# Optimization experiments

Measured on AMD Instinct MI355X. Metric: run time of the kernel, lower is better.

## Reference

```python
import jax, jax.numpy as jnp
import numpy as np

B, S, D = 2, 2048, 1024
H, DH = 16, 64
N_CTX = 2048
IGNORE = -100000.0


def setup_inputs() -> dict:
    key = jax.random.key(0)
    ks = jax.random.split(key, 6)
    scale = 0.02
    return {
        "x": jax.random.normal(ks[0], (B, S, D), dtype=jnp.float32),
        "W_Q": jax.random.normal(ks[1], (H, DH, D), dtype=jnp.float32) * scale,
        "W_K": jax.random.normal(ks[2], (H, DH, D), dtype=jnp.float32) * scale,
        "W_V": jax.random.normal(ks[3], (H, DH, D), dtype=jnp.float32) * scale,
        "W_O": jax.random.normal(ks[4], (H, D, DH), dtype=jnp.float32) * scale,
        "b_Q": jnp.zeros((H, DH), dtype=jnp.float32),
        "b_K": jnp.zeros((H, DH), dtype=jnp.float32),
        "b_V": jnp.zeros((H, DH), dtype=jnp.float32),
        "b_O": jnp.zeros((D,), dtype=jnp.float32),
    }


def reference(x, W_Q, W_K, W_V, W_O, b_Q, b_K, b_V, b_O):
    attn_scale = jnp.sqrt(jnp.asarray(DH, dtype=x.dtype))
    # q,k,v: [batch, pos, head, d_head]
    q = jnp.einsum('ihm,bpm->bpih', W_Q, x) + b_Q
    k = jnp.einsum('ihm,bpm->bpih', W_K, x) + b_K
    v = jnp.einsum('ihm,bpm->bpih', W_V, x) + b_V
    # scores: [batch, head, q_pos, k_pos]
    attn_scores = jnp.einsum('bpih,bqih->bipq', q, k) / attn_scale
    # causal mask (pos_start=0, no kv cache)
    qs, ks_ = attn_scores.shape[-2], attn_scores.shape[-1]
    mask = jnp.tril(jnp.ones((qs, ks_), dtype=bool))
    attn_scores = jnp.where(mask, attn_scores, jnp.asarray(IGNORE, dtype=attn_scores.dtype))
    attn_matrix = jax.nn.softmax(attn_scores, axis=-1)
    # z: [batch, q_pos, head, d_head]
    z = jnp.einsum('bpih,biqp->bqih', v, attn_matrix)
    out = jnp.einsum('idh,bqih->bqd', W_O, z) + b_O
    return out
```

## Files before the change

kernel.cpp:

```cpp
#include <hip/hip_runtime.h>

typedef __bf16 bf16;
typedef __bf16 bf16x4 __attribute__((ext_vector_type(4)));
typedef __bf16 bf16x8 __attribute__((ext_vector_type(8)));
typedef float f32x4 __attribute__((ext_vector_type(4)));
typedef unsigned u32x4 __attribute__((ext_vector_type(4)));

#define AS1C(p) ((const __attribute__((address_space(1))) void*)(p))
#define AS3(p)  ((__attribute__((address_space(3))) void*)(p))

__device__ __forceinline__ void gld16(const bf16* gsrc, bf16* ldst) {
  __builtin_amdgcn_global_load_lds(AS1C(gsrc), AS3(ldst), 16, 0, 0);
}


__global__ void castx_kernel(const float* __restrict__ x, bf16* __restrict__ xb) {
  const int n4 = (4096 * 1024) / 4;
  for (int i = blockIdx.x * blockDim.x + threadIdx.x; i < n4; i += gridDim.x * blockDim.x) {
    float4 v = ((const float4*)x)[i];
    bf16x4 o;
    o[0] = (bf16)v.x; o[1] = (bf16)v.y; o[2] = (bf16)v.z; o[3] = (bf16)v.w;
    ((bf16x4*)xb)[i] = o;
  }
}

__global__ void prep_kernel(const float* __restrict__ WQ, const float* __restrict__ WK,
                            const float* __restrict__ WV, const float* __restrict__ WO,
                            const float* __restrict__ bQ, const float* __restrict__ bK,
                            const float* __restrict__ bV,
                            bf16* __restrict__ Wqkv, bf16* __restrict__ Wo2,
                            float* __restrict__ biasq) {
  const int WN = 1024 * 1024;
  const int total = 4 * WN + 3072;
  for (int i = blockIdx.x * blockDim.x + threadIdx.x; i < total; i += gridDim.x * blockDim.x) {
    if (i < WN) {
      Wqkv[i] = (bf16)(WQ[i] * 0.125f);
    } else if (i < 2 * WN) {
      Wqkv[i] = (bf16)WK[i - WN];
    } else if (i < 3 * WN) {
      Wqkv[i] = (bf16)WV[i - 2 * WN];
    } else if (i < 4 * WN) {
      int j = i - 3 * WN;
      int hh = j >> 16, r = j & 65535, d = r >> 6, dh = r & 63;
      Wo2[d * 1024 + hh * 64 + dh] = (bf16)WO[j];
    } else {
      int n = i - 4 * WN;
      biasq[n] = (n < 1024) ? bQ[n] * 0.125f : (n < 2048) ? bK[n - 1024] : bV[n - 2048];
    }
  }
}

template <int MODE>
__global__ __launch_bounds__(256)
void gemm_bt(const bf16* __restrict__ A, const bf16* __restrict__ Bw,
             const float* __restrict__ bias,
             bf16* __restrict__ Qo, bf16* __restrict__ Ko, bf16* __restrict__ Vt,
             float* __restrict__ Co, int M, int N, int K) {
  __shared__ bf16 As[128 * 64];
  __shared__ bf16 Bs[128 * 64];
  const int tid = threadIdx.x;
  const int lane = tid & 63, w = tid >> 6;
  const int wr = w >> 1, wc = w & 1;
  const int g = lane >> 4, lr = lane & 15;
  const int brow = blockIdx.x * 128, bcol = blockIdx.y * 128;

  f32x4 acc[4][4] = {};

  for (int k0 = 0; k0 < K; k0 += 64) {
#pragma unroll
    for (int it = 0; it < 4; ++it) {
      const int chunk = it * 4 + w;
      const int e = chunk * 64 + lane;
      const int row = e >> 3;
      const int c8 = (e & 7) << 3;
      gld16(A + (size_t)(brow + row) * K + k0 + c8, As + chunk * 512);
      gld16(Bw + (size_t)(bcol + row) * K + k0 + c8, Bs + chunk * 512);
    }
    __syncthreads();
#pragma unroll
    for (int kk = 0; kk < 2; ++kk) {
      bf16x8 af[4], bfm[4];
#pragma unroll
      for (int m = 0; m < 4; ++m)
        af[m] = *(const bf16x8*)(As + (wr * 64 + m * 16 + lr) * 64 + kk * 32 + g * 8);
#pragma unroll
      for (int n = 0; n < 4; ++n)
        bfm[n] = *(const bf16x8*)(Bs + (wc * 64 + n * 16 + lr) * 64 + kk * 32 + g * 8);
#pragma unroll
      for (int m = 0; m < 4; ++m)
#pragma unroll
        for (int n = 0; n < 4; ++n)
          acc[m][n] = __builtin_amdgcn_mfma_f32_16x16x32_bf16(af[m], bfm[n], acc[m][n], 0, 0, 0);
    }
    __syncthreads();
  }

  const int row0 = brow + wr * 64;
  const int col0 = bcol + wc * 64;
#pragma unroll
  for (int m = 0; m < 4; ++m) {
#pragma unroll
    for (int n = 0; n < 4; ++n) {
      const int nidx = col0 + n * 16 + lr;
      f32x4 v = acc[m][n];
      const float bs = bias[nidx];
      if (MODE == 0) {
        const int stream = nidx >> 10;
        const int j = nidx & 1023;
        const int hh = j >> 6, dh = j & 63;
        const int r0 = row0 + m * 16 + g * 4;
        const int b = r0 >> 11;
        const int p0 = r0 & 2047;
        if (stream == 2) {
          bf16x4 vv;
#pragma unroll
          for (int i = 0; i < 4; ++i) vv[i] = (bf16)(v[i] + bs);
          *(bf16x4*)(Vt + ((size_t)(b * 16 + hh) * 64 + dh) * 2048 + p0) = vv;
        } else {
          bf16* dst = (stream == 0) ? Qo : Ko;
#pragma unroll
          for (int i = 0; i < 4; ++i)
            dst[((size_t)(b * 16 + hh) * 2048 + (p0 + i)) * 64 + dh] = (bf16)(v[i] + bs);
        }
      } else {
#pragma unroll
        for (int i = 0; i < 4; ++i) {
          const int r = row0 + m * 16 + g * 4 + i;
          Co[(size_t)r * 1024 + nidx] = v[i] + bs;
        }
      }
    }
  }
}

__global__ __launch_bounds__(256, 4)
void attn_kernel(const bf16* __restrict__ Qm, const bf16* __restrict__ Km,
                 const bf16* __restrict__ Vm, bf16* __restrict__ Z) {
  const int nblk = blockIdx.x;
  const int xcd = nblk & 7, slot = nblk >> 3;
  const int G = ((slot >> 5) << 3) + xcd;
  const int qt = slot & 31;
  const int hh = G & 15, b = G >> 4;
  const int bh = b * 16 + hh;
  const int lane = threadIdx.x & 63, w = threadIdx.x >> 6;
  const int g = lane >> 4, lr = lane & 15;
  const bool g0 = g & 1, g1 = (g >> 1) & 1;

  __shared__ bf16 Ks[2][4096];
  __shared__ bf16 Vs[2][4096];

  const bf16* Qb = Qm + (size_t)bh * 2048 * 64;
  const bf16* Kb = Km + (size_t)bh * 2048 * 64;
  const bf16* Vb = Vm + (size_t)bh * 64 * 2048;

  auto stage = [&](int kv0, int bufi) {
#pragma unroll
    for (int it = 0; it < 2; ++it) {
      const int cb = w * 128 + it * 64;
      const int u = cb + lane;
      const int lc = u ^ ((u >> 3) & 7);
      const int row = lc >> 3, c8 = (lc & 7) * 8;
      gld16(Kb + (size_t)(kv0 + row) * 64 + c8, &Ks[bufi][cb * 8]);
      gld16(Vb + (size_t)row * 2048 + kv0 + c8, &Vs[bufi][cb * 8]);
    }
  };

  const int q0w = qt * 64 + w * 16;
  const int qg = q0w + lr;

  bf16x8 aq[2];
#pragma unroll
  for (int kk = 0; kk < 2; ++kk)
    aq[kk] = *(const bf16x8*)(Qb + (size_t)qg * 64 + kk * 32 + g * 8);

  float m_i = -1e30f, l_i = 0.f;
  f32x4 oacc[4] = {};

  stage(0, 0);
  __syncthreads();
  int buf = 0;

  for (int t = 0; t <= qt; ++t) {
    if (t < qt) stage((t + 1) * 64, buf ^ 1);
    const int kv0 = t * 64;

    f32x4 s[4] = {};
#pragma unroll
    for (int kk = 0; kk < 2; ++kk) {
#pragma unroll
      for (int n = 0; n < 4; ++n) {
        const int r = n * 16 + lr;
        const int sl = (r * 8 + kk * 4 + g) ^ (r & 7);
        bf16x8 bk = *(const bf16x8*)(&Ks[buf][sl * 8]);
        s[n] = __builtin_amdgcn_mfma_f32_16x16x32_bf16(bk, aq[kk], s[n], 0, 0, 0);
      }
    }
    if (t == qt) {
#pragma unroll
      for (int n = 0; n < 4; ++n)
#pragma unroll
        for (int i = 0; i < 4; ++i)
          if (kv0 + n * 16 + g * 4 + i > qg) s[n][i] = -1e9f;
    }

    float tm = fmaxf(fmaxf(fmaxf(s[0][0], s[0][1]), fmaxf(s[0][2], s[0][3])),
                     fmaxf(fmaxf(s[1][0], s[1][1]), fmaxf(s[1][2], s[1][3])));
    tm = fmaxf(tm, fmaxf(fmaxf(fmaxf(s[2][0], s[2][1]), fmaxf(s[2][2], s[2][3])),
                         fmaxf(fmaxf(s[3][0], s[3][1]), fmaxf(s[3][2], s[3][3]))));
    tm = fmaxf(tm, __shfl_xor(tm, 16));
    tm = fmaxf(tm, __shfl_xor(tm, 32));
    const float mn = fmaxf(m_i, tm);
    const float al = __expf(m_i - mn);
    m_i = mn;
#pragma unroll
    for (int n = 0; n < 4; ++n)
#pragma unroll
      for (int i = 0; i < 4; ++i) s[n][i] = __expf(s[n][i] - mn);
    float ts = ((s[0][0] + s[0][1]) + (s[0][2] + s[0][3])) +
               ((s[1][0] + s[1][1]) + (s[1][2] + s[1][3])) +
               ((s[2][0] + s[2][1]) + (s[2][2] + s[2][3])) +
               ((s[3][0] + s[3][1]) + (s[3][2] + s[3][3]));
    ts += __shfl_xor(ts, 16);
    ts += __shfl_xor(ts, 32);
    l_i = l_i * al + ts;
#pragma unroll
    for (int n = 0; n < 4; ++n)
#pragma unroll
      for (int i = 0; i < 4; ++i) oacc[n][i] *= al;

    unsigned U[8];
#pragma unroll
    for (int n = 0; n < 4; ++n)
#pragma unroll
      for (int h = 0; h < 2; ++h) {
        unsigned lo = (unsigned)__builtin_bit_cast(unsigned short, (bf16)s[n][2 * h]);
        unsigned hi = (unsigned)__builtin_bit_cast(unsigned short, (bf16)s[n][2 * h + 1]);
        U[n * 2 + h] = lo | (hi << 16);
      }
    unsigned rA0 = (unsigned)__shfl_xor((int)(g1 ? U[0] : U[2]), 32);
    unsigned rA1 = (unsigned)__shfl_xor((int)(g1 ? U[1] : U[3]), 32);
    unsigned rA2 = (unsigned)__shfl_xor((int)(g1 ? U[4] : U[6]), 32);
    unsigned rA3 = (unsigned)__shfl_xor((int)(g1 ? U[5] : U[7]), 32);
    unsigned v2_000 = g1 ? rA0 : U[0];
    unsigned v2_001 = g1 ? rA1 : U[1];
    unsigned v2_010 = g1 ? U[2] : rA0;
    unsigned v2_011 = g1 ? U[3] : rA1;
    unsigned v2_100 = g1 ? rA2 : U[4];
    unsigned v2_101 = g1 ? rA3 : U[5];
    unsigned v2_110 = g1 ? U[6] : rA2;
    unsigned v2_111 = g1 ? U[7] : rA3;
    unsigned rB0 = (unsigned)__shfl_xor((int)(g0 ? v2_000 : v2_010), 16);
    unsigned rB1 = (unsigned)__shfl_xor((int)(g0 ? v2_001 : v2_011), 16);
    unsigned rB2 = (unsigned)__shfl_xor((int)(g0 ? v2_100 : v2_110), 16);
    unsigned rB3 = (unsigned)__shfl_xor((int)(g0 ? v2_101 : v2_111), 16);
    u32x4 t0, t1;
    t0[0] = g0 ? rB0 : v2_000;
    t0[1] = g0 ? rB1 : v2_001;
    t0[2] = g0 ? v2_010 : rB0;
    t0[3] = g0 ? v2_011 : rB1;
    t1[0] = g0 ? rB2 : v2_100;
    t1[1] = g0 ? rB3 : v2_101;
    t1[2] = g0 ? v2_110 : rB2;
    t1[3] = g0 ? v2_111 : rB3;
    bf16x8 pb0 = __builtin_bit_cast(bf16x8, t0);
    bf16x8 pb1 = __builtin_bit_cast(bf16x8, t1);

#pragma unroll
    for (int kk = 0; kk < 2; ++kk) {
      const bf16x8 pb = kk ? pb1 : pb0;
#pragma unroll
      for (int n = 0; n < 4; ++n) {
        const int r = n * 16 + lr;
        const int sl = (r * 8 + kk * 4 + g) ^ (r & 7);
        bf16x8 av = *(const bf16x8*)(&Vs[buf][sl * 8]);
        oacc[n] = __builtin_amdgcn_mfma_f32_16x16x32_bf16(av, pb, oacc[n], 0, 0, 0);
      }
    }
    __syncthreads();
    buf ^= 1;
  }

  const float li = 1.f / l_i;
  bf16* zrow = Z + ((size_t)(b * 2048 + qg) * 16 + hh) * 64;
#pragma unroll
  for (int n = 0; n < 4; ++n) {
    bf16x4 o4;
#pragma unroll
    for (int i = 0; i < 4; ++i) o4[i] = (bf16)(oacc[n][i] * li);
    *(bf16x4*)(zrow + n * 16 + g * 4) = o4;
  }
}

extern "C" void kernel_launch(void* const* d_in, const int* in_sizes, int n_in,
                              void* d_out, int out_size, void* d_ws, size_t ws_size,
                              hipStream_t stream) {
  const float* x  = (const float*)d_in[0];
  const float* WQ = (const float*)d_in[1];
  const float* WK = (const float*)d_in[2];
  const float* WV = (const float*)d_in[3];
  const float* WO = (const float*)d_in[4];
  const float* bQ = (const float*)d_in[5];
  const float* bK = (const float*)d_in[6];
  const float* bV = (const float*)d_in[7];
  const float* bO = (const float*)d_in[8];
  float* out = (float*)d_out;

  char* ws = (char*)d_ws;
  bf16* xb    = (bf16*)(ws);
  bf16* Wqkv  = (bf16*)(ws + (8u << 20));
  bf16* Wo2   = (bf16*)(ws + (14u << 20));
  bf16* Qb    = (bf16*)(ws + (16u << 20));
  bf16* Kb    = (bf16*)(ws + (24u << 20));
  bf16* Vtb   = (bf16*)(ws + (32u << 20));
  bf16* Zb    = (bf16*)(ws + (40u << 20));
  float* biasq = (float*)(ws + (48u << 20));

  castx_kernel<<<2048, 256, 0, stream>>>(x, xb);
  prep_kernel<<<2048, 256, 0, stream>>>(WQ, WK, WV, WO, bQ, bK, bV, Wqkv, Wo2, biasq);
  gemm_bt<0><<<dim3(32, 24), 256, 0, stream>>>(xb, Wqkv, biasq, Qb, Kb, Vtb, nullptr,
                                               4096, 3072, 1024);
  attn_kernel<<<1024, 256, 0, stream>>>(Qb, Kb, Vtb, Zb);
  gemm_bt<1><<<dim3(32, 8), 256, 0, stream>>>(Zb, Wo2, bO, nullptr, nullptr, nullptr, out,
                                              4096, 1024, 1024);
}
```

Baseline: 243.9 us.

## Split long causal attention rows across two blocks and merge with combine kernel

Query tiles in the upper half of the causal range (qt ≥ 16) now have their KV loop split into two halves run by separate blocks. Each half writes an unnormalized partial output plus (max, sum) statistics, and a new combine kernel merges them into Z. Blocks are also scheduled heaviest-first, so the longest block runs 16 tiles instead of 32, which targets the load-imbalance tail of the causal kernel. In exchange it adds an extra kernel launch and partial-result traffic. The partials reuse workspace regions (xb, Wqkv) that are already consumed by that point.

```diff
diff --git a/kernel.cpp b/kernel.cpp
--- a/kernel.cpp
+++ b/kernel.cpp
@@ -135,30 +135,39 @@
 
 __global__ __launch_bounds__(256, 4)
 void attn_kernel(const bf16* __restrict__ Qm, const bf16* __restrict__ Km,
-                 const bf16* __restrict__ Vm, bf16* __restrict__ Z) {
+                 const bf16* __restrict__ Vm, bf16* __restrict__ Z,
+                 bf16* __restrict__ OP, float2* __restrict__ ML) {
   const int nblk = blockIdx.x;
-  const int xcd = nblk & 7, slot = nblk >> 3;
-  const int G = ((slot >> 5) << 3) + xcd;
-  const int qt = slot & 31;
+  const int xcd = nblk & 7, s2 = nblk >> 3;
+  const int Gl = s2 & 3, u = s2 >> 2;
+  const int G = Gl * 8 + xcd;
   const int hh = G & 15, b = G >> 4;
-  const int bh = b * 16 + hh;
   const int lane = threadIdx.x & 63, w = threadIdx.x >> 6;
   const int g = lane >> 4, lr = lane & 15;
   const bool g0 = g & 1, g1 = (g >> 1) & 1;
 
+  int qt, t0, t1, spl;
+  if (u < 32) {
+    qt = 31 - (u >> 1); spl = u & 1;
+    const int T = qt + 1, mid = (T + 1) >> 1;
+    t0 = spl ? mid : 0; t1 = spl ? T : mid;
+  } else {
+    qt = 47 - u; spl = -1; t0 = 0; t1 = qt + 1;
+  }
+
   __shared__ bf16 Ks[2][4096];
   __shared__ bf16 Vs[2][4096];
 
-  const bf16* Qb = Qm + (size_t)bh * 2048 * 64;
-  const bf16* Kb = Km + (size_t)bh * 2048 * 64;
-  const bf16* Vb = Vm + (size_t)bh * 64 * 2048;
+  const bf16* Qb = Qm + (size_t)G * 2048 * 64;
+  const bf16* Kb = Km + (size_t)G * 2048 * 64;
+  const bf16* Vb = Vm + (size_t)G * 64 * 2048;
 
   auto stage = [&](int kv0, int bufi) {
 #pragma unroll
     for (int it = 0; it < 2; ++it) {
       const int cb = w * 128 + it * 64;
-      const int u = cb + lane;
-      const int lc = u ^ ((u >> 3) & 7);
+      const int uu = cb + lane;
+      const int lc = uu ^ ((uu >> 3) & 7);
       const int row = lc >> 3, c8 = (lc & 7) * 8;
       gld16(Kb + (size_t)(kv0 + row) * 64 + c8, &Ks[bufi][cb * 8]);
       gld16(Vb + (size_t)row * 2048 + kv0 + c8, &Vs[bufi][cb * 8]);
@@ -176,12 +185,12 @@
   float m_i = -1e30f, l_i = 0.f;
   f32x4 oacc[4] = {};
 
-  stage(0, 0);
+  int buf = 0;
+  stage(t0 * 64, 0);
   __syncthreads();
-  int buf = 0;
-
-  for (int t = 0; t <= qt; ++t) {
-    if (t < qt) stage((t + 1) * 64, buf ^ 1);
+
+  for (int t = t0; t < t1; ++t) {
+    if (t + 1 < t1) stage((t + 1) * 64, buf ^ 1);
     const int kv0 = t * 64;
 
     f32x4 s[4] = {};
@@ -253,17 +262,17 @@
     unsigned rB1 = (unsigned)__shfl_xor((int)(g0 ? v2_001 : v2_011), 16);
     unsigned rB2 = (unsigned)__shfl_xor((int)(g0 ? v2_100 : v2_110), 16);
     unsigned rB3 = (unsigned)__shfl_xor((int)(g0 ? v2_101 : v2_111), 16);
-    u32x4 t0, t1;
-    t0[0] = g0 ? rB0 : v2_000;
-    t0[1] = g0 ? rB1 : v2_001;
-    t0[2] = g0 ? v2_010 : rB0;
-    t0[3] = g0 ? v2_011 : rB1;
-    t1[0] = g0 ? rB2 : v2_100;
-    t1[1] = g0 ? rB3 : v2_101;
-    t1[2] = g0 ? v2_110 : rB2;
-    t1[3] = g0 ? v2_111 : rB3;
-    bf16x8 pb0 = __builtin_bit_cast(bf16x8, t0);
-    bf16x8 pb1 = __builtin_bit_cast(bf16x8, t1);
+    u32x4 t0v, t1v;
+    t0v[0] = g0 ? rB0 : v2_000;
+    t0v[1] = g0 ? rB1 : v2_001;
+    t0v[2] = g0 ? v2_010 : rB0;
+    t0v[3] = g0 ? v2_011 : rB1;
+    t1v[0] = g0 ? rB2 : v2_100;
+    t1v[1] = g0 ? rB3 : v2_101;
+    t1v[2] = g0 ? v2_110 : rB2;
+    t1v[3] = g0 ? v2_111 : rB3;
+    bf16x8 pb0 = __builtin_bit_cast(bf16x8, t0v);
+    bf16x8 pb1 = __builtin_bit_cast(bf16x8, t1v);
 
 #pragma unroll
     for (int kk = 0; kk < 2; ++kk) {
@@ -280,15 +289,48 @@
     buf ^= 1;
   }
 
-  const float li = 1.f / l_i;
-  bf16* zrow = Z + ((size_t)(b * 2048 + qg) * 16 + hh) * 64;
-#pragma unroll
-  for (int n = 0; n < 4; ++n) {
-    bf16x4 o4;
-#pragma unroll
-    for (int i = 0; i < 4; ++i) o4[i] = (bf16)(oacc[n][i] * li);
-    *(bf16x4*)(zrow + n * 16 + g * 4) = o4;
-  }
+  if (u < 32) {
+    const int pr = G * 1024 + (qt - 16) * 64 + w * 16 + lr;
+    bf16* oprow = OP + (size_t)(spl * 32768 + pr) * 64;
+#pragma unroll
+    for (int n = 0; n < 4; ++n) {
+      bf16x4 o4;
+#pragma unroll
+      for (int i = 0; i < 4; ++i) o4[i] = (bf16)oacc[n][i];
+      *(bf16x4*)(oprow + n * 16 + g * 4) = o4;
+    }
+    if (lane < 16) ML[spl * 32768 + pr] = make_float2(m_i, l_i);
+  } else {
+    const float li = 1.f / l_i;
+    bf16* zrow = Z + ((size_t)(b * 2048 + qg) * 16 + hh) * 64;
+#pragma unroll
+    for (int n = 0; n < 4; ++n) {
+      bf16x4 o4;
+#pragma unroll
+      for (int i = 0; i < 4; ++i) o4[i] = (bf16)(oacc[n][i] * li);
+      *(bf16x4*)(zrow + n * 16 + g * 4) = o4;
+    }
+  }
+}
+
+__global__ __launch_bounds__(256)
+void combine_kernel(const bf16* __restrict__ OP, const float2* __restrict__ ML,
+                    bf16* __restrict__ Z) {
+  const int id = blockIdx.x * 256 + threadIdx.x;
+  const int pr = id >> 3, d8 = id & 7;
+  const float2 ml0 = ML[pr], ml1 = ML[32768 + pr];
+  const float m = fmaxf(ml0.x, ml1.x);
+  const float w0 = __expf(ml0.x - m), w1 = __expf(ml1.x - m);
+  const float inv = 1.f / (ml0.y * w0 + ml1.y * w1);
+  const bf16x8 a = *(const bf16x8*)(OP + (size_t)pr * 64 + d8 * 8);
+  const bf16x8 c = *(const bf16x8*)(OP + ((size_t)32768 + pr) * 64 + d8 * 8);
+  bf16x8 o;
+#pragma unroll
+  for (int j = 0; j < 8; ++j)
+    o[j] = (bf16)(((float)a[j] * w0 + (float)c[j] * w1) * inv);
+  const int bh = pr >> 10, qr = pr & 1023;
+  const int bb = bh >> 4, hq = bh & 15;
+  *(bf16x8*)(Z + (((size_t)(bb * 2048 + 1024 + qr)) * 16 + hq) * 64 + d8 * 8) = o;
 }
 
 extern "C" void kernel_launch(void* const* d_in, const int* in_sizes, int n_in,
@@ -314,12 +356,15 @@
   bf16* Vtb   = (bf16*)(ws + (32u << 20));
   bf16* Zb    = (bf16*)(ws + (40u << 20));
   float* biasq = (float*)(ws + (48u << 20));
+  bf16* OP    = (bf16*)(ws);
+  float2* ML  = (float2*)(ws + (8u << 20));
 
   castx_kernel<<<2048, 256, 0, stream>>>(x, xb);
   prep_kernel<<<2048, 256, 0, stream>>>(WQ, WK, WV, WO, bQ, bK, bV, Wqkv, Wo2, biasq);
   gemm_bt<0><<<dim3(32, 24), 256, 0, stream>>>(xb, Wqkv, biasq, Qb, Kb, Vtb, nullptr,
                                                4096, 3072, 1024);
-  attn_kernel<<<1024, 256, 0, stream>>>(Qb, Kb, Vtb, Zb);
+  attn_kernel<<<1536, 256, 0, stream>>>(Qb, Kb, Vtb, Zb, OP, ML);
+  combine_kernel<<<1024, 256, 0, stream>>>(OP, ML, Zb);
   gemm_bt<1><<<dim3(32, 8), 256, 0, stream>>>(Zb, Wo2, bO, nullptr, nullptr, nullptr, out,
                                               4096, 1024, 1024);
 }
```

After: 221.5 us. 1.1x faster.
